# Kernel optimization log

Hardware: AMD Instinct MI355X
Metric: run time of the kernel (lower is better)

## Reference

```python
import math
import jax, jax.numpy as jnp
import numpy as np

B, C, H, W = 4, 64, 128, 128
A = 64           # attention_size
OUT = 64         # output_size
KS = 3           # kernel_size
M = (KS - 1) // 2
SCALE = A ** (-0.5)


def _lin(x, Wt, b):
    return x @ Wt + b


def _pos_encoding(d_model, seq_len):
    # sinusoidal PE over the k^2 neighborhood positions; d_model even here
    pos = jnp.arange(seq_len, dtype=jnp.float32)[:, None]
    div = jnp.exp(jnp.arange(0, d_model, 2, dtype=jnp.float32) * (-math.log(10000.0) / d_model))
    s = jnp.sin(pos * div)   # (seq, d/2)
    c = jnp.cos(pos * div)
    return jnp.stack([s, c], axis=-1).reshape(seq_len, d_model)  # interleaved sin/cos


def _expand_shift(k_nchw):
    # k_nchw: (b, c, h, w) -> (b, c, h, w, KS*KS) neighbor gather (zero padded)
    h, w = k_nchw.shape[2], k_nchw.shape[3]
    p = jnp.pad(k_nchw, ((0, 0), (0, 0), (M, M), (M, M)))
    slices = [p[:, :, i:i + h, j:j + w] for i in range(KS) for j in range(KS)]
    return jnp.stack(slices, axis=-1)


def setup_inputs() -> dict:
    key = jax.random.key(0)
    ks = jax.random.split(key, 12)
    sd = lambda fan_in: 1.0 / math.sqrt(fan_in)
    return {
        "x": jax.random.normal(ks[0], (B, C, H, W), jnp.float32),
        "ln_g": jnp.ones((C,), jnp.float32),
        "ln_b": jnp.zeros((C,), jnp.float32),
        "Wq": jax.random.normal(ks[1], (C, 2 * A), jnp.float32) * sd(C),
        "bq": jnp.zeros((2 * A,), jnp.float32),
        "Wq2": jax.random.normal(ks[2], (2 * A, A), jnp.float32) * sd(2 * A),
        "bq2": jnp.zeros((A,), jnp.float32),
        "Wk": jax.random.normal(ks[3], (C, 2 * A), jnp.float32) * sd(C),
        "bk": jnp.zeros((2 * A,), jnp.float32),
        "Wk2": jax.random.normal(ks[4], (2 * A, A), jnp.float32) * sd(2 * A),
        "bk2": jnp.zeros((A,), jnp.float32),
        "Wv": jax.random.normal(ks[5], (C, 2 * A), jnp.float32) * sd(C),
        "bv": jnp.zeros((2 * A,), jnp.float32),
        "Wv2": jax.random.normal(ks[6], (2 * A, OUT), jnp.float32) * sd(2 * A),
        "bv2": jnp.zeros((OUT,), jnp.float32),
        "Wpos": jax.random.normal(ks[7], (C, A), jnp.float32) * sd(C),
        "bpos": jnp.zeros((A,), jnp.float32),
        "Wposk": jax.random.normal(ks[8], (A, A), jnp.float32) * sd(A),
        "bposk": jnp.zeros((A,), jnp.float32),
    }


def reference(x, ln_g, ln_b, Wq, bq, Wq2, bq2, Wk, bk, Wk2, bk2,
              Wv, bv, Wv2, bv2, Wpos, bpos, Wposk, bposk):
    # positional embedding over the 9 neighborhood slots
    pe = _pos_encoding(C, KS * KS)                       # (9, C)
    pos_emb = jax.nn.relu(_lin(pe, Wpos, bpos))          # (9, A)

    xn = jnp.transpose(x, (0, 2, 3, 1))                  # (b, h, w, c)
    mu = jnp.mean(xn, axis=-1, keepdims=True)
    var = jnp.mean((xn - mu) ** 2, axis=-1, keepdims=True)
    xn = (xn - mu) * jax.lax.rsqrt(var + 1e-5) * ln_g + ln_b

    K = _lin(jax.nn.relu(_lin(xn, Wk, bk)), Wk2, bk2)    # (b, h, w, A)
    Ksh = _expand_shift(jnp.transpose(K, (0, 3, 1, 2)))  # (b, A, h, w, 9)
    pos_k = jnp.transpose(_lin(pos_emb, Wposk, bposk))   # (A, 9)
    Kfull = Ksh + pos_k[None, :, None, None, :]

    Q = _lin(jax.nn.relu(_lin(xn, Wq, bq)), Wq2, bq2)    # (b, h, w, A)
    V = _lin(jax.nn.relu(_lin(xn, Wv, bv)), Wv2, bv2)    # (b, h, w, OUT)
    Vsh = _expand_shift(jnp.transpose(V, (0, 3, 1, 2)))  # (b, OUT, h, w, 9)

    att = jnp.einsum('bhwa,bahwp->bphw', Q, Kfull) * SCALE
    att = jax.nn.softmax(att, axis=1)                    # softmax over 9 neighbors
    out = jnp.einsum('bchwn,bnhw->bchw', Vsh, att)       # (b, OUT, h, w)
    return out  # stride == 1 -> no subsampling
```

## Files before the change

kernel.cpp:

```cpp
#include <hip/hip_runtime.h>
#include <hip/hip_bf16.h>
#include <math.h>

typedef __attribute__((ext_vector_type(8))) short short8;
typedef __attribute__((ext_vector_type(4))) float float4v;
typedef unsigned short ushort_t;
typedef unsigned int uint_t;

#define HWPIX 16384
#define NPIX  65536

__device__ inline float b2f(ushort_t u) {
    uint_t x = ((uint_t)u) << 16;
    return __builtin_bit_cast(float, x);
}
__device__ inline ushort_t f2b(float f) {
    uint_t x = __builtin_bit_cast(uint_t, f);
    uint_t r = (x + 0x7fffu + ((x >> 16) & 1u)) >> 16;
    return (ushort_t)r;
}
__device__ inline uint_t pack2(float a, float b) {
    return (uint_t)f2b(a) | ((uint_t)f2b(b) << 16);
}
__device__ inline bool probe_bf16(const void* lng) {
    return *(const uint_t*)lng == 0x3F803F80u;
}
__device__ inline float ldf(const void* p, int i, bool bf) {
    return bf ? b2f(((const ushort_t*)p)[i]) : ((const float*)p)[i];
}
__device__ inline float lo2f(uint_t u) { return __builtin_bit_cast(float, u << 16); }
__device__ inline float hi2f(uint_t u) { return __builtin_bit_cast(float, u & 0xffff0000u); }
__device__ inline void unpack8(uint4 u, float* f) {
    f[0] = lo2f(u.x); f[1] = hi2f(u.x);
    f[2] = lo2f(u.y); f[3] = hi2f(u.y);
    f[4] = lo2f(u.z); f[5] = hi2f(u.z);
    f[6] = lo2f(u.w); f[7] = hi2f(u.w);
}

__global__ __launch_bounds__(256) void prep_kernel(
        const void* __restrict__ Wq, const void* __restrict__ Wq2,
        const void* __restrict__ Wk, const void* __restrict__ Wk2,
        const void* __restrict__ Wv, const void* __restrict__ Wv2,
        const void* __restrict__ Wpos, const void* __restrict__ bpos,
        const void* __restrict__ Wposk, const void* __restrict__ bposk,
        const void* __restrict__ lng,
        ushort_t* __restrict__ W1A, ushort_t* __restrict__ W2A, ushort_t* __restrict__ pkA) {
    bool bf = probe_bf16(lng);
    if (blockIdx.x < 96) {
        int idx = blockIdx.x * 256 + threadIdx.x;
        int chain = idx >> 13;
        int o = idx & 8191;
        const void* W1 = chain == 0 ? Wq : (chain == 1 ? Wk : Wv);
        const void* W2 = chain == 0 ? Wq2 : (chain == 1 ? Wk2 : Wv2);
        {
            int j = o & 7, L = (o >> 3) & 63, kc = (o >> 9) & 1, mt = (o >> 10) & 7;
            int k = kc * 32 + ((L >> 4) << 3) + j;
            int m = mt * 16 + (L & 15);
            W1A[chain * 8192 + o] = f2b(ldf(W1, k * 128 + m, bf));
        }
        {
            int j = o & 7, L = (o >> 3) & 63, kc = (o >> 9) & 3, mt2 = (o >> 11) & 3;
            int k = kc * 32 + ((L >> 4) << 3) + j;
            int m = mt2 * 16 + (L & 15);
            W2A[chain * 8192 + o] = f2b(ldf(W2, k * 64 + m, bf));
        }
    } else {
        __shared__ float pe[9][64];
        __shared__ float pemb[9][64];
        __shared__ float pks[64][9];
        int t = threadIdx.x;
        for (int it = t; it < 576; it += 256) {
            int p = it >> 6, a = it & 63;
            int i = a >> 1;
            float div = expf(-(float)(2 * i) * 0.14391156831212787f);
            float ang = (float)p * div;
            pe[p][a] = (a & 1) ? cosf(ang) : sinf(ang);
        }
        __syncthreads();
        for (int it = t; it < 576; it += 256) {
            int p = it >> 6, a = it & 63;
            float s = ldf(bpos, a, bf);
            for (int c = 0; c < 64; ++c) s += pe[p][c] * ldf(Wpos, c * 64 + a, bf);
            pemb[p][a] = fmaxf(s, 0.f);
        }
        __syncthreads();
        for (int it = t; it < 576; it += 256) {
            int p = it >> 6, a = it & 63;
            float s = ldf(bposk, a, bf);
            for (int j = 0; j < 64; ++j) s += pemb[p][j] * ldf(Wposk, j * 64 + a, bf);
            pks[a][p] = s;
        }
        __syncthreads();
        if (t < 128) {
            int kc = t >> 6, L = t & 63;
            int m = L & 15;
#pragma unroll
            for (int j = 0; j < 8; ++j) {
                int k = kc * 32 + ((L >> 4) << 3) + j;
                pkA[(kc * 64 + L) * 8 + j] = (m < 9) ? f2b(pks[k][m]) : (ushort_t)0;
            }
        }
    }
}

__global__ __launch_bounds__(256) void lnqkv_kernel(
        const void* __restrict__ x, const void* __restrict__ g, const void* __restrict__ bb,
        const ushort_t* __restrict__ W1A, const ushort_t* __restrict__ W2A,
        const ushort_t* __restrict__ pkAp,
        const void* __restrict__ b1q, const void* __restrict__ b1k, const void* __restrict__ b1v,
        const void* __restrict__ b2q, const void* __restrict__ b2k, const void* __restrict__ b2v,
        const void* __restrict__ lng,
        ushort_t* __restrict__ Qo, ushort_t* __restrict__ Ko, ushort_t* __restrict__ Vo,
        float* __restrict__ Spos) {
    bool bf = probe_bf16(lng);
    int tid = threadIdx.x;
    int wave = tid >> 6, lane = tid & 63;
    int q = lane >> 4, r = lane & 15;
    int base = blockIdx.x * 128 + wave * 32;
    int b = base >> 14;
    int spBase = base & 16383;

    short8 pkA0 = *reinterpret_cast<const short8*>(pkAp + (0 * 64 + lane) * 8);
    short8 pkA1 = *reinterpret_cast<const short8*>(pkAp + (1 * 64 + lane) * 8);

    short8 bfr[2][2];
#pragma unroll
    for (int t = 0; t < 2; ++t) {
        int sp = spBase + t * 16 + r;
        float xl[8], xh[8];
        if (bf) {
            const ushort_t* xb = (const ushort_t*)x + (size_t)b * 64 * HWPIX + sp;
#pragma unroll
            for (int j = 0; j < 8; ++j) {
                xl[j] = b2f(xb[(size_t)(q * 8 + j) * HWPIX]);
                xh[j] = b2f(xb[(size_t)(32 + q * 8 + j) * HWPIX]);
            }
        } else {
            const float* xb = (const float*)x + (size_t)b * 64 * HWPIX + sp;
#pragma unroll
            for (int j = 0; j < 8; ++j) {
                xl[j] = xb[(size_t)(q * 8 + j) * HWPIX];
                xh[j] = xb[(size_t)(32 + q * 8 + j) * HWPIX];
            }
        }
        float s1 = 0.f, s2 = 0.f;
#pragma unroll
        for (int j = 0; j < 8; ++j) {
            s1 += xl[j] + xh[j];
            s2 += xl[j] * xl[j] + xh[j] * xh[j];
        }
        s1 += __shfl_xor(s1, 16); s2 += __shfl_xor(s2, 16);
        s1 += __shfl_xor(s1, 32); s2 += __shfl_xor(s2, 32);
        float mu = s1 * (1.f / 64.f);
        float var = s2 * (1.f / 64.f) - mu * mu;
        float rstd = rsqrtf(var + 1e-5f);
#pragma unroll
        for (int j = 0; j < 8; ++j) {
            int c = q * 8 + j;
            bfr[t][0][j] = (short)f2b((xl[j] - mu) * rstd * ldf(g, c, bf) + ldf(bb, c, bf));
            bfr[t][1][j] = (short)f2b((xh[j] - mu) * rstd * ldf(g, c + 32, bf) + ldf(bb, c + 32, bf));
        }
    }

    __shared__ __align__(16) ushort_t hid[4][2][16][128];

#pragma unroll 1
    for (int chain = 0; chain < 3; ++chain) {
        const ushort_t* W1 = W1A + chain * 8192;
        const ushort_t* W2 = W2A + chain * 8192;
        const void* b1 = chain == 0 ? b1q : (chain == 1 ? b1k : b1v);
        const void* b2 = chain == 0 ? b2q : (chain == 1 ? b2k : b2v);
        ushort_t* out = chain == 0 ? Qo : (chain == 1 ? Ko : Vo);

        {
            short8 w1[8][2];
#pragma unroll
            for (int mt = 0; mt < 8; ++mt)
#pragma unroll
                for (int kc = 0; kc < 2; ++kc)
                    w1[mt][kc] = *reinterpret_cast<const short8*>(W1 + ((mt * 2 + kc) * 64 + lane) * 8);
#pragma unroll
            for (int mt = 0; mt < 8; ++mt) {
                float bias0 = ldf(b1, mt * 16 + q * 4 + 0, bf);
                float bias1 = ldf(b1, mt * 16 + q * 4 + 1, bf);
                float bias2 = ldf(b1, mt * 16 + q * 4 + 2, bf);
                float bias3 = ldf(b1, mt * 16 + q * 4 + 3, bf);
#pragma unroll
                for (int t = 0; t < 2; ++t) {
                    float4v acc = {0.f, 0.f, 0.f, 0.f};
                    acc = __builtin_amdgcn_mfma_f32_16x16x32_bf16(w1[mt][0], bfr[t][0], acc, 0, 0, 0);
                    acc = __builtin_amdgcn_mfma_f32_16x16x32_bf16(w1[mt][1], bfr[t][1], acc, 0, 0, 0);
                    float v0 = fmaxf(acc[0] + bias0, 0.f);
                    float v1 = fmaxf(acc[1] + bias1, 0.f);
                    float v2 = fmaxf(acc[2] + bias2, 0.f);
                    float v3 = fmaxf(acc[3] + bias3, 0.f);
                    int chunk = (2 * mt + (q >> 1)) ^ r;
                    ushort_t* dst = &hid[wave][t][r][0] + chunk * 8 + (q & 1) * 4;
                    uint2 d; d.x = pack2(v0, v1); d.y = pack2(v2, v3);
                    *reinterpret_cast<uint2*>(dst) = d;
                }
            }
        }
        {
            short8 w2[4][4];
#pragma unroll
            for (int mt2 = 0; mt2 < 4; ++mt2)
#pragma unroll
                for (int kc = 0; kc < 4; ++kc)
                    w2[mt2][kc] = *reinterpret_cast<const short8*>(W2 + ((mt2 * 4 + kc) * 64 + lane) * 8);
            short8 h2[2][4];
#pragma unroll
            for (int t = 0; t < 2; ++t)
#pragma unroll
                for (int kc = 0; kc < 4; ++kc) {
                    int chunk = (4 * kc + q) ^ r;
                    h2[t][kc] = *reinterpret_cast<const short8*>(&hid[wave][t][r][0] + chunk * 8);
                }
#pragma unroll
            for (int mt2 = 0; mt2 < 4; ++mt2) {
                float bias0 = ldf(b2, mt2 * 16 + q * 4 + 0, bf);
                float bias1 = ldf(b2, mt2 * 16 + q * 4 + 1, bf);
                float bias2 = ldf(b2, mt2 * 16 + q * 4 + 2, bf);
                float bias3 = ldf(b2, mt2 * 16 + q * 4 + 3, bf);
#pragma unroll
                for (int t = 0; t < 2; ++t) {
                    float4v acc = {0.f, 0.f, 0.f, 0.f};
#pragma unroll
                    for (int kc = 0; kc < 4; ++kc)
                        acc = __builtin_amdgcn_mfma_f32_16x16x32_bf16(w2[mt2][kc], h2[t][kc], acc, 0, 0, 0);
                    uint2 d;
                    d.x = pack2(acc[0] + bias0, acc[1] + bias1);
                    d.y = pack2(acc[2] + bias2, acc[3] + bias3);
                    int pixel = base + t * 16 + r;
                    *reinterpret_cast<uint2*>(out + (size_t)pixel * 64 + mt2 * 16 + q * 4) = d;
                    if (chain == 0) {
                        int chunk = (2 * mt2 + (q >> 1)) ^ r;
                        ushort_t* dst = &hid[wave][t][r][0] + chunk * 8 + (q & 1) * 4;
                        *reinterpret_cast<uint2*>(dst) = d;
                    }
                }
            }
        }
        if (chain == 0) {
#pragma unroll
            for (int t = 0; t < 2; ++t) {
                short8 qB0, qB1;
                {
                    int chunk = (4 * 0 + q) ^ r;
                    qB0 = *reinterpret_cast<const short8*>(&hid[wave][t][r][0] + chunk * 8);
                }
                {
                    int chunk = (4 * 1 + q) ^ r;
                    qB1 = *reinterpret_cast<const short8*>(&hid[wave][t][r][0] + chunk * 8);
                }
                float4v acc = {0.f, 0.f, 0.f, 0.f};
                acc = __builtin_amdgcn_mfma_f32_16x16x32_bf16(pkA0, qB0, acc, 0, 0, 0);
                acc = __builtin_amdgcn_mfma_f32_16x16x32_bf16(pkA1, qB1, acc, 0, 0, 0);
                int pixel = base + t * 16 + r;
                float4 o;
                o.x = acc[0]; o.y = acc[1]; o.z = acc[2]; o.w = acc[3];
                *reinterpret_cast<float4*>(Spos + (size_t)pixel * 16 + q * 4) = o;
            }
        }
    }
}

__global__ __launch_bounds__(256) void attn_kernel(
        const ushort_t* __restrict__ Q, const ushort_t* __restrict__ K,
        const ushort_t* __restrict__ V, const float* __restrict__ Spos,
        const void* __restrict__ lng, void* __restrict__ out) {
    bool bf = probe_bf16(lng);
    int p = blockIdx.x * 256 + threadIdx.x;
    int b = p >> 14;
    int sp = p & 16383;
    int h = sp >> 7, w = sp & 127;

    float v64[64];
    const ushort_t* qp = Q + (size_t)p * 64;
#pragma unroll
    for (int c0 = 0; c0 < 64; c0 += 8) {
        uint4 u = *reinterpret_cast<const uint4*>(qp + c0);
        unpack8(u, &v64[c0]);
    }

    float s[9];
    {
        float4 s0 = *reinterpret_cast<const float4*>(Spos + (size_t)p * 16);
        float4 s1 = *reinterpret_cast<const float4*>(Spos + (size_t)p * 16 + 4);
        s[0] = s0.x; s[1] = s0.y; s[2] = s0.z; s[3] = s0.w;
        s[4] = s1.x; s[5] = s1.y; s[6] = s1.z; s[7] = s1.w;
        s[8] = Spos[(size_t)p * 16 + 8];
    }
#pragma unroll
    for (int n = 0; n < 9; ++n) {
        int dy = n / 3 - 1, dx = n % 3 - 1;
        int hh = h + dy, ww = w + dx;
        float dot = 0.f;
        if (hh >= 0 && hh < 128 && ww >= 0 && ww < 128) {
            const ushort_t* kp = K + ((size_t)(b << 14) + (size_t)(hh * 128 + ww)) * 64;
#pragma unroll
            for (int c0 = 0; c0 < 64; c0 += 8) {
                uint4 u = *reinterpret_cast<const uint4*>(kp + c0);
                float kv[8];
                unpack8(u, kv);
#pragma unroll
                for (int j = 0; j < 8; ++j) dot += v64[c0 + j] * kv[j];
            }
        }
        s[n] = (s[n] + dot) * 0.125f;
    }
    float m = s[0];
#pragma unroll
    for (int n = 1; n < 9; ++n) m = fmaxf(m, s[n]);
    float sum = 0.f;
#pragma unroll
    for (int n = 0; n < 9; ++n) { s[n] = expf(s[n] - m); sum += s[n]; }
    float inv = 1.f / sum;

#pragma unroll
    for (int c = 0; c < 64; ++c) v64[c] = 0.f;
#pragma unroll
    for (int n = 0; n < 9; ++n) {
        int dy = n / 3 - 1, dx = n % 3 - 1;
        int hh = h + dy, ww = w + dx;
        if (hh < 0 || hh >= 128 || ww < 0 || ww >= 128) continue;
        float a = s[n] * inv;
        const ushort_t* vp = V + ((size_t)(b << 14) + (size_t)(hh * 128 + ww)) * 64;
#pragma unroll
        for (int c0 = 0; c0 < 64; c0 += 8) {
            uint4 u = *reinterpret_cast<const uint4*>(vp + c0);
            float vv[8];
            unpack8(u, vv);
#pragma unroll
            for (int j = 0; j < 8; ++j) v64[c0 + j] += a * vv[j];
        }
    }
    if (bf) {
        ushort_t* ob = (ushort_t*)out + ((size_t)b * 64) * HWPIX + sp;
#pragma unroll
        for (int c = 0; c < 64; ++c) ob[(size_t)c * HWPIX] = f2b(v64[c]);
    } else {
        float* ob = (float*)out + ((size_t)b * 64) * HWPIX + sp;
#pragma unroll
        for (int c = 0; c < 64; ++c) ob[(size_t)c * HWPIX] = v64[c];
    }
}

extern "C" void kernel_launch(void* const* d_in, const int* in_sizes, int n_in,
                              void* d_out, int out_size, void* d_ws, size_t ws_size,
                              hipStream_t stream) {
    (void)in_sizes; (void)n_in; (void)out_size; (void)ws_size;
    const void* x     = d_in[0];
    const void* ln_g  = d_in[1];
    const void* ln_b  = d_in[2];
    const void* Wq    = d_in[3];
    const void* bq    = d_in[4];
    const void* Wq2   = d_in[5];
    const void* bq2   = d_in[6];
    const void* Wk    = d_in[7];
    const void* bk    = d_in[8];
    const void* Wk2   = d_in[9];
    const void* bk2   = d_in[10];
    const void* Wv    = d_in[11];
    const void* bv    = d_in[12];
    const void* Wv2   = d_in[13];
    const void* bv2   = d_in[14];
    const void* Wpos  = d_in[15];
    const void* bpos  = d_in[16];
    const void* Wposk = d_in[17];
    const void* bposk = d_in[18];

    char* ws = (char*)d_ws;
    ushort_t* Qo   = (ushort_t*)(ws);
    ushort_t* Ko   = (ushort_t*)(ws + (size_t)8 * 1024 * 1024);
    ushort_t* Vo   = (ushort_t*)(ws + (size_t)16 * 1024 * 1024);
    float*    Spos = (float*)(ws + (size_t)24 * 1024 * 1024);
    ushort_t* W1A  = (ushort_t*)(ws + (size_t)28 * 1024 * 1024);
    ushort_t* W2A  = (ushort_t*)(ws + (size_t)28 * 1024 * 1024 + 65536);
    ushort_t* pkA  = (ushort_t*)(ws + (size_t)28 * 1024 * 1024 + 131072);

    prep_kernel<<<97, 256, 0, stream>>>(Wq, Wq2, Wk, Wk2, Wv, Wv2,
                                        Wpos, bpos, Wposk, bposk, ln_g, W1A, W2A, pkA);
    lnqkv_kernel<<<512, 256, 0, stream>>>(x, ln_g, ln_b, W1A, W2A, pkA,
                                          bq, bk, bv, bq2, bk2, bv2, ln_g, Qo, Ko, Vo, Spos);
    attn_kernel<<<256, 256, 0, stream>>>(Qo, Ko, Vo, Spos, ln_g, d_out);
}
```

Baseline: 176.0 us.

## Halve pixels per wave in LN+QKV kernel and shrink attention blocks for more parallelism

The LN+QKV kernel now has each wave handle one 16-pixel tile instead of two, with twice as many blocks. Weight fragments are loaded inside the MFMA loops rather than held in large register arrays, and the shared hidden buffer is halved. The attention kernel switches to 128-thread blocks with twice as many blocks, which spreads the 65536 pixels across more CUs. The aim is higher occupancy and less register pressure, at the cost of reloading weights more often per pixel and fewer MFMAs in flight per wave.

```diff
diff --git a/kernel.cpp b/kernel.cpp
--- a/kernel.cpp
+++ b/kernel.cpp
@@ -116,17 +116,15 @@
     int tid = threadIdx.x;
     int wave = tid >> 6, lane = tid & 63;
     int q = lane >> 4, r = lane & 15;
-    int base = blockIdx.x * 128 + wave * 32;
+    int base = blockIdx.x * 64 + wave * 16;
     int b = base >> 14;
-    int spBase = base & 16383;
+    int sp = (base & 16383) + r;
 
     short8 pkA0 = *reinterpret_cast<const short8*>(pkAp + (0 * 64 + lane) * 8);
     short8 pkA1 = *reinterpret_cast<const short8*>(pkAp + (1 * 64 + lane) * 8);
 
-    short8 bfr[2][2];
-#pragma unroll
-    for (int t = 0; t < 2; ++t) {
-        int sp = spBase + t * 16 + r;
+    short8 bfr0, bfr1;
+    {
         float xl[8], xh[8];
         if (bf) {
             const ushort_t* xb = (const ushort_t*)x + (size_t)b * 64 * HWPIX + sp;
@@ -157,12 +155,12 @@
 #pragma unroll
         for (int j = 0; j < 8; ++j) {
             int c = q * 8 + j;
-            bfr[t][0][j] = (short)f2b((xl[j] - mu) * rstd * ldf(g, c, bf) + ldf(bb, c, bf));
-            bfr[t][1][j] = (short)f2b((xh[j] - mu) * rstd * ldf(g, c + 32, bf) + ldf(bb, c + 32, bf));
-        }
-    }
-
-    __shared__ __align__(16) ushort_t hid[4][2][16][128];
+            bfr0[j] = (short)f2b((xl[j] - mu) * rstd * ldf(g, c, bf) + ldf(bb, c, bf));
+            bfr1[j] = (short)f2b((xh[j] - mu) * rstd * ldf(g, c + 32, bf) + ldf(bb, c + 32, bf));
+        }
+    }
+
+    __shared__ __align__(16) ushort_t hid[4][16][128];
 
 #pragma unroll 1
     for (int chain = 0; chain < 3; ++chain) {
@@ -172,105 +170,65 @@
         const void* b2 = chain == 0 ? b2q : (chain == 1 ? b2k : b2v);
         ushort_t* out = chain == 0 ? Qo : (chain == 1 ? Ko : Vo);
 
-        {
-            short8 w1[8][2];
-#pragma unroll
-            for (int mt = 0; mt < 8; ++mt)
-#pragma unroll
-                for (int kc = 0; kc < 2; ++kc)
-                    w1[mt][kc] = *reinterpret_cast<const short8*>(W1 + ((mt * 2 + kc) * 64 + lane) * 8);
-#pragma unroll
-            for (int mt = 0; mt < 8; ++mt) {
-                float bias0 = ldf(b1, mt * 16 + q * 4 + 0, bf);
-                float bias1 = ldf(b1, mt * 16 + q * 4 + 1, bf);
-                float bias2 = ldf(b1, mt * 16 + q * 4 + 2, bf);
-                float bias3 = ldf(b1, mt * 16 + q * 4 + 3, bf);
-#pragma unroll
-                for (int t = 0; t < 2; ++t) {
-                    float4v acc = {0.f, 0.f, 0.f, 0.f};
-                    acc = __builtin_amdgcn_mfma_f32_16x16x32_bf16(w1[mt][0], bfr[t][0], acc, 0, 0, 0);
-                    acc = __builtin_amdgcn_mfma_f32_16x16x32_bf16(w1[mt][1], bfr[t][1], acc, 0, 0, 0);
-                    float v0 = fmaxf(acc[0] + bias0, 0.f);
-                    float v1 = fmaxf(acc[1] + bias1, 0.f);
-                    float v2 = fmaxf(acc[2] + bias2, 0.f);
-                    float v3 = fmaxf(acc[3] + bias3, 0.f);
-                    int chunk = (2 * mt + (q >> 1)) ^ r;
-                    ushort_t* dst = &hid[wave][t][r][0] + chunk * 8 + (q & 1) * 4;
-                    uint2 d; d.x = pack2(v0, v1); d.y = pack2(v2, v3);
-                    *reinterpret_cast<uint2*>(dst) = d;
-                }
-            }
-        }
-        {
-            short8 w2[4][4];
-#pragma unroll
-            for (int mt2 = 0; mt2 < 4; ++mt2)
-#pragma unroll
-                for (int kc = 0; kc < 4; ++kc)
-                    w2[mt2][kc] = *reinterpret_cast<const short8*>(W2 + ((mt2 * 4 + kc) * 64 + lane) * 8);
-            short8 h2[2][4];
-#pragma unroll
-            for (int t = 0; t < 2; ++t)
-#pragma unroll
-                for (int kc = 0; kc < 4; ++kc) {
-                    int chunk = (4 * kc + q) ^ r;
-                    h2[t][kc] = *reinterpret_cast<const short8*>(&hid[wave][t][r][0] + chunk * 8);
-                }
-#pragma unroll
-            for (int mt2 = 0; mt2 < 4; ++mt2) {
-                float bias0 = ldf(b2, mt2 * 16 + q * 4 + 0, bf);
-                float bias1 = ldf(b2, mt2 * 16 + q * 4 + 1, bf);
-                float bias2 = ldf(b2, mt2 * 16 + q * 4 + 2, bf);
-                float bias3 = ldf(b2, mt2 * 16 + q * 4 + 3, bf);
-#pragma unroll
-                for (int t = 0; t < 2; ++t) {
-                    float4v acc = {0.f, 0.f, 0.f, 0.f};
-#pragma unroll
-                    for (int kc = 0; kc < 4; ++kc)
-                        acc = __builtin_amdgcn_mfma_f32_16x16x32_bf16(w2[mt2][kc], h2[t][kc], acc, 0, 0, 0);
-                    uint2 d;
-                    d.x = pack2(acc[0] + bias0, acc[1] + bias1);
-                    d.y = pack2(acc[2] + bias2, acc[3] + bias3);
-                    int pixel = base + t * 16 + r;
-                    *reinterpret_cast<uint2*>(out + (size_t)pixel * 64 + mt2 * 16 + q * 4) = d;
-                    if (chain == 0) {
-                        int chunk = (2 * mt2 + (q >> 1)) ^ r;
-                        ushort_t* dst = &hid[wave][t][r][0] + chunk * 8 + (q & 1) * 4;
-                        *reinterpret_cast<uint2*>(dst) = d;
-                    }
-                }
+#pragma unroll
+        for (int mt = 0; mt < 8; ++mt) {
+            short8 w10 = *reinterpret_cast<const short8*>(W1 + ((mt * 2 + 0) * 64 + lane) * 8);
+            short8 w11 = *reinterpret_cast<const short8*>(W1 + ((mt * 2 + 1) * 64 + lane) * 8);
+            float4v acc = {0.f, 0.f, 0.f, 0.f};
+            acc = __builtin_amdgcn_mfma_f32_16x16x32_bf16(w10, bfr0, acc, 0, 0, 0);
+            acc = __builtin_amdgcn_mfma_f32_16x16x32_bf16(w11, bfr1, acc, 0, 0, 0);
+            float v0 = fmaxf(acc[0] + ldf(b1, mt * 16 + q * 4 + 0, bf), 0.f);
+            float v1 = fmaxf(acc[1] + ldf(b1, mt * 16 + q * 4 + 1, bf), 0.f);
+            float v2 = fmaxf(acc[2] + ldf(b1, mt * 16 + q * 4 + 2, bf), 0.f);
+            float v3 = fmaxf(acc[3] + ldf(b1, mt * 16 + q * 4 + 3, bf), 0.f);
+            int chunk = (2 * mt + (q >> 1)) ^ r;
+            uint2 d; d.x = pack2(v0, v1); d.y = pack2(v2, v3);
+            *reinterpret_cast<uint2*>(&hid[wave][r][chunk * 8 + (q & 1) * 4]) = d;
+        }
+        short8 h2[4];
+#pragma unroll
+        for (int kc = 0; kc < 4; ++kc)
+            h2[kc] = *reinterpret_cast<const short8*>(&hid[wave][r][((4 * kc + q) ^ r) * 8]);
+#pragma unroll
+        for (int mt2 = 0; mt2 < 4; ++mt2) {
+            float4v acc = {0.f, 0.f, 0.f, 0.f};
+#pragma unroll
+            for (int kc = 0; kc < 4; ++kc) {
+                short8 w2 = *reinterpret_cast<const short8*>(W2 + ((mt2 * 4 + kc) * 64 + lane) * 8);
+                acc = __builtin_amdgcn_mfma_f32_16x16x32_bf16(w2, h2[kc], acc, 0, 0, 0);
+            }
+            uint2 d;
+            d.x = pack2(acc[0] + ldf(b2, mt2 * 16 + q * 4 + 0, bf),
+                        acc[1] + ldf(b2, mt2 * 16 + q * 4 + 1, bf));
+            d.y = pack2(acc[2] + ldf(b2, mt2 * 16 + q * 4 + 2, bf),
+                        acc[3] + ldf(b2, mt2 * 16 + q * 4 + 3, bf));
+            int pixel = base + r;
+            *reinterpret_cast<uint2*>(out + (size_t)pixel * 64 + mt2 * 16 + q * 4) = d;
+            if (chain == 0) {
+                int chunk = (2 * mt2 + (q >> 1)) ^ r;
+                *reinterpret_cast<uint2*>(&hid[wave][r][chunk * 8 + (q & 1) * 4]) = d;
             }
         }
         if (chain == 0) {
-#pragma unroll
-            for (int t = 0; t < 2; ++t) {
-                short8 qB0, qB1;
-                {
-                    int chunk = (4 * 0 + q) ^ r;
-                    qB0 = *reinterpret_cast<const short8*>(&hid[wave][t][r][0] + chunk * 8);
-                }
-                {
-                    int chunk = (4 * 1 + q) ^ r;
-                    qB1 = *reinterpret_cast<const short8*>(&hid[wave][t][r][0] + chunk * 8);
-                }
-                float4v acc = {0.f, 0.f, 0.f, 0.f};
-                acc = __builtin_amdgcn_mfma_f32_16x16x32_bf16(pkA0, qB0, acc, 0, 0, 0);
-                acc = __builtin_amdgcn_mfma_f32_16x16x32_bf16(pkA1, qB1, acc, 0, 0, 0);
-                int pixel = base + t * 16 + r;
-                float4 o;
-                o.x = acc[0]; o.y = acc[1]; o.z = acc[2]; o.w = acc[3];
-                *reinterpret_cast<float4*>(Spos + (size_t)pixel * 16 + q * 4) = o;
-            }
-        }
-    }
-}
-
-__global__ __launch_bounds__(256) void attn_kernel(
+            short8 qB0 = *reinterpret_cast<const short8*>(&hid[wave][r][((4 * 0 + q) ^ r) * 8]);
+            short8 qB1 = *reinterpret_cast<const short8*>(&hid[wave][r][((4 * 1 + q) ^ r) * 8]);
+            float4v acc = {0.f, 0.f, 0.f, 0.f};
+            acc = __builtin_amdgcn_mfma_f32_16x16x32_bf16(pkA0, qB0, acc, 0, 0, 0);
+            acc = __builtin_amdgcn_mfma_f32_16x16x32_bf16(pkA1, qB1, acc, 0, 0, 0);
+            int pixel = base + r;
+            float4 o;
+            o.x = acc[0]; o.y = acc[1]; o.z = acc[2]; o.w = acc[3];
+            *reinterpret_cast<float4*>(Spos + (size_t)pixel * 16 + q * 4) = o;
+        }
+    }
+}
+
+__global__ __launch_bounds__(128) void attn_kernel(
         const ushort_t* __restrict__ Q, const ushort_t* __restrict__ K,
         const ushort_t* __restrict__ V, const float* __restrict__ Spos,
         const void* __restrict__ lng, void* __restrict__ out) {
     bool bf = probe_bf16(lng);
-    int p = blockIdx.x * 256 + threadIdx.x;
+    int p = blockIdx.x * 128 + threadIdx.x;
     int b = p >> 14;
     int sp = p & 16383;
     int h = sp >> 7, w = sp & 127;
@@ -381,7 +339,7 @@
 
     prep_kernel<<<97, 256, 0, stream>>>(Wq, Wq2, Wk, Wk2, Wv, Wv2,
                                         Wpos, bpos, Wposk, bposk, ln_g, W1A, W2A, pkA);
-    lnqkv_kernel<<<512, 256, 0, stream>>>(x, ln_g, ln_b, W1A, W2A, pkA,
-                                          bq, bk, bv, bq2, bk2, bv2, ln_g, Qo, Ko, Vo, Spos);
-    attn_kernel<<<256, 256, 0, stream>>>(Qo, Ko, Vo, Spos, ln_g, d_out);
-}
+    lnqkv_kernel<<<1024, 256, 0, stream>>>(x, ln_g, ln_b, W1A, W2A, pkA,
+                                           bq, bk, bv, bq2, bk2, bv2, ln_g, Qo, Ko, Vo, Spos);
+    attn_kernel<<<512, 128, 0, stream>>>(Qo, Ko, Vo, Spos, ln_g, d_out);
+}
```

Measured after the change: 174.7 us. About the same (-0.7%).
